# Optimization experiments

Measured on AMD Instinct MI355X. Metric: run time of the kernel, lower is better.

Reference implementation:

```python
import jax, jax.numpy as jnp
import numpy as np

N_EXPERTS = 64
TOPK = 4
DIM = 2048
B_T = 8192


def setup_inputs() -> dict:
    key = jax.random.key(0)
    k1, k2 = jax.random.split(key)
    x = jax.random.normal(k1, (B_T, DIM), jnp.float32)
    W = jax.random.normal(k2, (N_EXPERTS, DIM), jnp.float32) * 0.02  # nn.Linear weight (out, in)
    router_bias = jnp.zeros((N_EXPERTS,), jnp.float32)  # registered buffer, init zeros
    return {"x": x, "W": W, "router_bias": router_bias, "token_capacity": 3072}


def _route(x, W, router_bias, token_capacity):
    """Faithful serial greedy capacity-aware routing.

    Replicates the torch nested loop (k-major, token-minor order):
      - per step, pick argmax over the token's (mutated) logits among experts
        with remaining capacity;
      - full experts whose logit exceeds the chosen one get permanently set
        to -inf in that token's logit row (exactly what the inner while-style
        loop does);
      - if no expert has capacity, selected stays -1, weight 0, and the whole
        row becomes -inf (torch sets the top expert to -inf n_experts times).
    """
    logits0 = x @ W.T + router_bias                       # (N, E)
    scores = jax.nn.softmax(logits0, axis=-1)             # (N, E)
    cap = token_capacity // TOPK                          # python int
    remaining0 = jnp.full((N_EXPERTS,), float(cap), jnp.float32)
    N = x.shape[0]
    NEG = jnp.float32(-jnp.inf)

    def step(carry, i):
        logits, remaining = carry
        b = i % N                                         # token index (k-major order)
        row = logits[b]                                   # (E,)
        masked = jnp.where(remaining > 0, row, NEG)
        chosen = jnp.argmax(masked)
        ok = remaining[chosen] > 0                        # False only if all experts full
        sel = jnp.where(ok, chosen, -1).astype(jnp.int32)
        w = jnp.where(ok, scores[b, chosen], jnp.float32(0.0))
        full = remaining <= 0
        cval = row[chosen]
        # full experts 'above' the chosen one were visited and zapped to -inf
        new_row = jnp.where(ok,
                            jnp.where(full & (row > cval), NEG, row),
                            jnp.full_like(row, NEG))
        logits = logits.at[b].set(new_row)
        remaining = remaining.at[chosen].add(jnp.where(ok, jnp.float32(-1.0), jnp.float32(0.0)))
        return (logits, remaining), (sel, w)

    (_, _), (sel_f, w_f) = jax.lax.scan(step, (logits0, remaining0),
                                        jnp.arange(TOPK * N))
    selected = sel_f.reshape(TOPK, N).T                   # (N, TOPK)
    weights = w_f.reshape(TOPK, N).T                      # (N, TOPK)
    weights = weights / (weights.sum(axis=-1, keepdims=True) + 1e-8)
    return selected, weights


def reference(x, W, router_bias, token_capacity):
    return _route(x, W, router_bias, token_capacity)
```

## Files before the change

kernel.cpp:

```cpp
#include <hip/hip_runtime.h>
#include <math.h>

#define N_TOK 8192
#define DIM   2048
#define NE    64
#define TOPK  4
#define THETA 2e-3f
#define TPB   16
#define NBLK  (N_TOK / TPB)
#define HSTR  16

typedef short bf16x8 __attribute__((ext_vector_type(8)));
typedef float f32x4  __attribute__((ext_vector_type(4)));

#define OFF_LOGITS 0
#define OFF_MAXV   (OFF_LOGITS + N_TOK * NE)
#define OFF_DENOM  (OFF_MAXV + N_TOK)
#define OFF_HIST   (OFF_DENOM + N_TOK)
#define OFF_WH     (OFF_HIST + NE * HSTR)
#define OFF_WL     (OFF_WH + NE * DIM / 2)
#define OFF_WT     (OFF_WL + NE * DIM / 2)
#define OFF_WTMP   (OFF_WT + NE * DIM)

__device__ inline void cvt2(float a, float b, unsigned& hi, unsigned& lo) {
    const unsigned ua = __float_as_uint(a), ub = __float_as_uint(b);
    hi = __builtin_amdgcn_perm(ub, ua, 0x07060302u);
    const float ra = a - __uint_as_float(ua & 0xFFFF0000u);
    const float rb = b - __uint_as_float(ub & 0xFFFF0000u);
    lo = __builtin_amdgcn_perm(__float_as_uint(rb), __float_as_uint(ra), 0x07060302u);
}

union FragU { unsigned u[4]; bf16x8 v; uint4 q; };

__device__ inline void make_frags(const float4& p, const float4& q,
                                  bf16x8& hi, bf16x8& lo) {
    FragU H, L;
    cvt2(p.x, p.y, H.u[0], L.u[0]);
    cvt2(p.z, p.w, H.u[1], L.u[1]);
    cvt2(q.x, q.y, H.u[2], L.u[2]);
    cvt2(q.z, q.w, H.u[3], L.u[3]);
    hi = H.v; lo = L.v;
}

__global__ __launch_bounds__(256)
void k_wc(const float* __restrict__ W, unsigned short* __restrict__ wh2,
          unsigned short* __restrict__ wl2, float* __restrict__ wt,
          int* __restrict__ hist) {
    const int t = blockIdx.x * 256 + threadIdx.x;
    if (t < NE * HSTR) hist[t] = 0;
    const int l  = t & 63;
    const int grp = t >> 6;
    const int nt = grp & 3;
    const int kc = grp >> 2;
    const int e  = nt * 16 + (l & 15);
    const int k0 = kc * 32 + (l >> 4) * 8;

    const float4 p = *reinterpret_cast<const float4*>(W + (size_t)e * DIM + k0);
    const float4 q = *reinterpret_cast<const float4*>(W + (size_t)e * DIM + k0 + 4);
    FragU H, L;
    cvt2(p.x, p.y, H.u[0], L.u[0]);
    cvt2(p.z, p.w, H.u[1], L.u[1]);
    cvt2(q.x, q.y, H.u[2], L.u[2]);
    cvt2(q.z, q.w, H.u[3], L.u[3]);
    const size_t off = (size_t)grp * 512 + l * 8;
    *reinterpret_cast<uint4*>(wh2 + off) = H.q;
    *reinterpret_cast<uint4*>(wl2 + off) = L.q;

    wt[(size_t)(k0 + 0) * NE + e] = p.x;
    wt[(size_t)(k0 + 1) * NE + e] = p.y;
    wt[(size_t)(k0 + 2) * NE + e] = p.z;
    wt[(size_t)(k0 + 3) * NE + e] = p.w;
    wt[(size_t)(k0 + 4) * NE + e] = q.x;
    wt[(size_t)(k0 + 5) * NE + e] = q.y;
    wt[(size_t)(k0 + 6) * NE + e] = q.z;
    wt[(size_t)(k0 + 7) * NE + e] = q.w;
}

__global__ __launch_bounds__(512, 4)
void k_main(const float* __restrict__ x, const unsigned short* __restrict__ wh2,
            const unsigned short* __restrict__ wl2, const float* __restrict__ bias,
            const float* __restrict__ wt,
            float* __restrict__ logits, float* __restrict__ maxv,
            float* __restrict__ denomv, int* __restrict__ hist,
            float* __restrict__ out) {
    __shared__ float red[8][TPB][68];
    __shared__ float lbuf[TPB][68];
    __shared__ int   selS[TPB];
    __shared__ float wS[TPB];
    __shared__ short flagIdx[TPB];
    __shared__ int   flagCnt;

    const int tid = threadIdx.x;
    const int w   = tid >> 6;
    const int l   = tid & 63;
    const int t0  = blockIdx.x * TPB;
    const int m   = l & 15;
    const int g   = l >> 4;

    if (tid == 0) flagCnt = 0;

    const float* aP = x + (size_t)(t0 + m) * DIM + w * 32 + g * 8;
    const unsigned short* bh = wh2 + (size_t)w * 2048 + l * 8;
    const unsigned short* bl = wl2 + (size_t)w * 2048 + l * 8;

    f32x4 accA[4], accB[4];
    #pragma unroll
    for (int nt = 0; nt < 4; ++nt)
        #pragma unroll
        for (int r = 0; r < 4; ++r) { accA[nt][r] = 0.0f; accB[nt][r] = 0.0f; }

    #pragma unroll
    for (int win = 0; win < 8; ++win) {
        const float4 p = *reinterpret_cast<const float4*>(aP + win * 256);
        const float4 q = *reinterpret_cast<const float4*>(aP + win * 256 + 4);
        uint4 BH[4], BL[4];
        #pragma unroll
        for (int nt = 0; nt < 4; ++nt) {
            BH[nt] = *reinterpret_cast<const uint4*>(
                bh + (size_t)win * 16384 + nt * 512);
            BL[nt] = *reinterpret_cast<const uint4*>(
                bl + (size_t)win * 16384 + nt * 512);
        }

        bf16x8 ah, al;
        make_frags(p, q, ah, al);

        #pragma unroll
        for (int nt = 0; nt < 4; ++nt) {
            FragU b; b.q = BH[nt];
            accA[nt] = __builtin_amdgcn_mfma_f32_16x16x32_bf16(ah, b.v, accA[nt], 0, 0, 0);
            accB[nt] = __builtin_amdgcn_mfma_f32_16x16x32_bf16(al, b.v, accB[nt], 0, 0, 0);
        }
        #pragma unroll
        for (int nt = 0; nt < 4; ++nt) {
            FragU b; b.q = BL[nt];
            accB[nt] = __builtin_amdgcn_mfma_f32_16x16x32_bf16(ah, b.v, accB[nt], 0, 0, 0);
        }
    }

    #pragma unroll
    for (int nt = 0; nt < 4; ++nt)
        #pragma unroll
        for (int r = 0; r < 4; ++r)
            red[w][g * 4 + r][nt * 16 + m] = accA[nt][r] + accB[nt][r];
    __syncthreads();

    for (int e2 = tid; e2 < TPB * NE; e2 += 512) {
        const int t = e2 >> 6, e = e2 & 63;
        float s = red[0][t][e];
        #pragma unroll
        for (int ww = 1; ww < 8; ++ww) s += red[ww][t][e];
        s += bias[e];
        logits[(size_t)(t0 + t) * NE + e] = s;
        lbuf[t][e] = s;
    }
    __syncthreads();

    #pragma unroll
    for (int tt = 0; tt < 2; ++tt) {
        const int t = w * 2 + tt;
        const float lv = lbuf[t][l];
        float v1 = lv; int i1 = l; float v2 = -INFINITY;
        #pragma unroll
        for (int off = 32; off; off >>= 1) {
            const float ov1 = __shfl_xor(v1, off);
            const int   oi1 = __shfl_xor(i1, off);
            const float ov2 = __shfl_xor(v2, off);
            if (ov1 > v1 || (ov1 == v1 && oi1 < i1)) {
                v2 = fmaxf(v1, ov2); v1 = ov1; i1 = oi1;
            } else {
                v2 = fmaxf(v2, ov1);
            }
        }
        float s = expf(lv - v1);
        #pragma unroll
        for (int off = 32; off; off >>= 1) s += __shfl_xor(s, off);
        if (l == 0) {
            const int row = t0 + t;
            maxv[row]   = v1;
            denomv[row] = s;
            selS[t]     = i1;
            wS[t]       = 1.0f / s;
            if (v1 - v2 < THETA) {
                const int ix = atomicAdd(&flagCnt, 1);
                flagIdx[ix] = (short)t;
            }
        }
    }
    __syncthreads();

    const int nf = flagCnt;
    for (int fi = 0; fi < nf; ++fi) {
        const int tl  = flagIdx[fi];
        const int row = t0 + tl;
        const float* xr = x + (size_t)row * DIM + w * 256;
        const float* wb = wt + (size_t)(w * 256) * NE + l;
        float a0 = 0.0f, a1 = 0.0f;
        #pragma unroll 4
        for (int k = 0; k < 256; k += 8) {
            const float4 x0 = *reinterpret_cast<const float4*>(xr + k);
            const float4 x1 = *reinterpret_cast<const float4*>(xr + k + 4);
            a0 = fmaf(x0.x, wb[(size_t)(k + 0) * NE], a0);
            a0 = fmaf(x0.y, wb[(size_t)(k + 1) * NE], a0);
            a0 = fmaf(x0.z, wb[(size_t)(k + 2) * NE], a0);
            a0 = fmaf(x0.w, wb[(size_t)(k + 3) * NE], a0);
            a1 = fmaf(x1.x, wb[(size_t)(k + 4) * NE], a1);
            a1 = fmaf(x1.y, wb[(size_t)(k + 5) * NE], a1);
            a1 = fmaf(x1.z, wb[(size_t)(k + 6) * NE], a1);
            a1 = fmaf(x1.w, wb[(size_t)(k + 7) * NE], a1);
        }
        red[w][0][l] = a0 + a1;
        __syncthreads();
        if (w == 0) {
            float lg = bias[l];
            #pragma unroll
            for (int s2 = 0; s2 < 8; ++s2) lg += red[s2][0][l];
            logits[(size_t)row * NE + l] = lg;
            float v = lg; int idx = l;
            #pragma unroll
            for (int off = 32; off; off >>= 1) {
                const float ov = __shfl_xor(v, off);
                const int   oi = __shfl_xor(idx, off);
                if (ov > v || (ov == v && oi < idx)) { v = ov; idx = oi; }
            }
            float p = expf(lg - v);
            #pragma unroll
            for (int off = 32; off; off >>= 1) p += __shfl_xor(p, off);
            if (l == 0) {
                maxv[row]   = v;
                denomv[row] = p;
                selS[tl]    = idx;
                wS[tl]      = 1.0f / p;
            }
        }
        __syncthreads();
    }

    if (w == 0) {
        int cnt = 0;
        #pragma unroll
        for (int t = 0; t < TPB; ++t) cnt += (selS[t] == l) ? 1 : 0;
        if (cnt) atomicAdd(&hist[l * HSTR], cnt);
    }

    if (tid < TPB) {
        const int row = t0 + tid;
        const float se = (float)selS[tid];
        const float wv = wS[tid];
        const float wn = wv / (4.0f * wv + 1e-8f);
        *reinterpret_cast<float4*>(out + (size_t)row * 4) = make_float4(se, se, se, se);
        *reinterpret_cast<float4*>(out + (size_t)N_TOK * TOPK + (size_t)row * 4) =
            make_float4(wn, wn, wn, wn);
    }
}

__global__ __launch_bounds__(256)
void k_decide(const int* __restrict__ hist, const float* __restrict__ logits,
              const float* __restrict__ maxv, const float* __restrict__ denomv,
              const int* __restrict__ tc, float* __restrict__ out,
              float* __restrict__ wtmp) {
    __shared__ int flagS;
    const int tid = threadIdx.x;
    const int cap = tc[0] / TOPK;
    if (tid < NE) {
        const bool bad = (TOPK * hist[tid * HSTR] > cap);
        const unsigned long long mm = __ballot(bad);
        if (tid == 0) flagS = (mm == 0ull) ? 1 : 0;
    }
    __syncthreads();
    if (flagS) return;

    if (tid < 64) {
        const int e = tid;
        int rem = cap;
        for (int k = 0; k < TOPK; ++k) {
            for (int b = 0; b < N_TOK; ++b) {
                const float lg = logits[(size_t)b * NE + e];
                float v = (rem > 0) ? lg : -INFINITY;
                int idx = e;
                #pragma unroll
                for (int off = 32; off; off >>= 1) {
                    const float ov = __shfl_xor(v, off);
                    const int   oi = __shfl_xor(idx, off);
                    if (ov > v || (ov == v && oi < idx)) { v = ov; idx = oi; }
                }
                const bool ok = (v != -INFINITY);
                if (ok && e == idx) rem -= 1;
                const float lc = __shfl(lg, idx);
                if (e == 0) {
                    out[(size_t)b * TOPK + k]  = ok ? (float)idx : -1.0f;
                    wtmp[(size_t)b * TOPK + k] = ok ? expf(lc - maxv[b]) / denomv[b] : 0.0f;
                }
            }
        }
    }
    __syncthreads();
    for (int b = tid; b < N_TOK; b += 256) {
        const float w0 = wtmp[b * 4 + 0], w1_ = wtmp[b * 4 + 1];
        const float w2 = wtmp[b * 4 + 2], w3 = wtmp[b * 4 + 3];
        const float s = ((w0 + w1_) + w2) + w3 + 1e-8f;
        out[N_TOK * TOPK + b * 4 + 0] = w0 / s;
        out[N_TOK * TOPK + b * 4 + 1] = w1_ / s;
        out[N_TOK * TOPK + b * 4 + 2] = w2 / s;
        out[N_TOK * TOPK + b * 4 + 3] = w3 / s;
    }
}

extern "C" void kernel_launch(void* const* d_in, const int* in_sizes, int n_in,
                              void* d_out, int out_size, void* d_ws, size_t ws_size,
                              hipStream_t stream) {
    const float* x    = (const float*)d_in[0];
    const float* W    = (const float*)d_in[1];
    const float* bias = (const float*)d_in[2];
    const int*   tc   = (const int*)d_in[3];

    float* ws       = (float*)d_ws;
    float* logits   = ws + OFF_LOGITS;
    float* maxv     = ws + OFF_MAXV;
    float* denomv   = ws + OFF_DENOM;
    int*   hist     = (int*)(ws + OFF_HIST);
    unsigned short* wh2 = (unsigned short*)(ws + OFF_WH);
    unsigned short* wl2 = (unsigned short*)(ws + OFF_WL);
    float* wt       = ws + OFF_WT;
    float* wtmp     = ws + OFF_WTMP;
    float* out      = (float*)d_out;

    k_wc<<<NE * DIM / 8 / 256, 256, 0, stream>>>(W, wh2, wl2, wt, hist);
    k_main<<<NBLK, 512, 0, stream>>>(x, wh2, wl2, bias, wt, logits, maxv,
                                     denomv, hist, out);
    k_decide<<<1, 256, 0, stream>>>(hist, logits, maxv, denomv, tc, out, wtmp);
}
```

Baseline: 131.0 us.

## Stage x and W tiles in LDS via async global-to-LDS loads, 32 tokens per block

```diff
diff --git a/kernel.cpp b/kernel.cpp
--- a/kernel.cpp
+++ b/kernel.cpp
@@ -6,7 +6,7 @@
 #define NE    64
 #define TOPK  4
 #define THETA 2e-3f
-#define TPB   16
+#define TPB   32
 #define NBLK  (N_TOK / TPB)
 #define HSTR  16
 
@@ -76,89 +76,106 @@
     wt[(size_t)(k0 + 7) * NE + e] = q.w;
 }
 
-__global__ __launch_bounds__(512, 4)
+__global__ __launch_bounds__(512, 2)
 void k_main(const float* __restrict__ x, const unsigned short* __restrict__ wh2,
             const unsigned short* __restrict__ wl2, const float* __restrict__ bias,
             const float* __restrict__ wt,
             float* __restrict__ logits, float* __restrict__ maxv,
             float* __restrict__ denomv, int* __restrict__ hist,
             float* __restrict__ out) {
-    __shared__ float red[8][TPB][68];
+    __shared__ __align__(16) char smem[98304];
     __shared__ float lbuf[TPB][68];
+    __shared__ float part[8][68];
     __shared__ int   selS[TPB];
     __shared__ float wS[TPB];
     __shared__ short flagIdx[TPB];
     __shared__ int   flagCnt;
 
     const int tid = threadIdx.x;
-    const int w   = tid >> 6;
+    const int ww  = tid >> 6;
     const int l   = tid & 63;
     const int t0  = blockIdx.x * TPB;
     const int m   = l & 15;
     const int g   = l >> 4;
+    const int tg  = ww >> 2;
+    const int eg  = ww & 3;
 
     if (tid == 0) flagCnt = 0;
 
-    const float* aP = x + (size_t)(t0 + m) * DIM + w * 32 + g * 8;
-    const unsigned short* bh = wh2 + (size_t)w * 2048 + l * 8;
-    const unsigned short* bl = wl2 + (size_t)w * 2048 + l * 8;
-
-    f32x4 accA[4], accB[4];
+    auto stage = [&](int win) {
+        #pragma unroll
+        for (int j = 0; j < 12; ++j) {
+            const int dbase = ww * 12288 + j * 1024;
+            const int d = dbase + l * 16;
+            const char* src;
+            if (dbase < 32768) {
+                const int r = d >> 10;
+                const int s = ((d >> 4) & 63) ^ (r & 7);
+                src = (const char*)(x + (size_t)(t0 + r) * DIM + win * 256 + s * 4);
+            } else if (dbase < 65536) {
+                src = (const char*)wh2 + (size_t)win * 32768 + (d - 32768);
+            } else {
+                src = (const char*)wl2 + (size_t)win * 32768 + (d - 65536);
+            }
+            __builtin_amdgcn_global_load_lds(
+                (const __attribute__((address_space(1))) void*)src,
+                (__attribute__((address_space(3))) void*)(smem + dbase),
+                16, 0, 0);
+        }
+    };
+
+    stage(0);
+    asm volatile("s_waitcnt vmcnt(0)" ::: "memory");
+    __syncthreads();
+
+    f32x4 accA, accB;
     #pragma unroll
-    for (int nt = 0; nt < 4; ++nt)
-        #pragma unroll
-        for (int r = 0; r < 4; ++r) { accA[nt][r] = 0.0f; accB[nt][r] = 0.0f; }
-
-    #pragma unroll
+    for (int r = 0; r < 4; ++r) { accA[r] = 0.0f; accB[r] = 0.0f; }
+
+    const int   arow  = tg * 16 + m;
+    const char* aBase = smem + arow * 1024;
+    const int   axor  = arow & 7;
+    const char* bhB   = smem + 32768 + eg * 1024 + l * 16;
+
     for (int win = 0; win < 8; ++win) {
-        const float4 p = *reinterpret_cast<const float4*>(aP + win * 256);
-        const float4 q = *reinterpret_cast<const float4*>(aP + win * 256 + 4);
-        uint4 BH[4], BL[4];
-        #pragma unroll
-        for (int nt = 0; nt < 4; ++nt) {
-            BH[nt] = *reinterpret_cast<const uint4*>(
-                bh + (size_t)win * 16384 + nt * 512);
-            BL[nt] = *reinterpret_cast<const uint4*>(
-                bl + (size_t)win * 16384 + nt * 512);
-        }
-
-        bf16x8 ah, al;
-        make_frags(p, q, ah, al);
-
-        #pragma unroll
-        for (int nt = 0; nt < 4; ++nt) {
-            FragU b; b.q = BH[nt];
-            accA[nt] = __builtin_amdgcn_mfma_f32_16x16x32_bf16(ah, b.v, accA[nt], 0, 0, 0);
-            accB[nt] = __builtin_amdgcn_mfma_f32_16x16x32_bf16(al, b.v, accB[nt], 0, 0, 0);
-        }
-        #pragma unroll
-        for (int nt = 0; nt < 4; ++nt) {
-            FragU b; b.q = BL[nt];
-            accB[nt] = __builtin_amdgcn_mfma_f32_16x16x32_bf16(ah, b.v, accB[nt], 0, 0, 0);
-        }
-    }
-
-    #pragma unroll
-    for (int nt = 0; nt < 4; ++nt)
+        #pragma unroll
+        for (int kc = 0; kc < 8; ++kc) {
+            const int s0 = kc * 8 + g * 2;
+            const float4 p = *reinterpret_cast<const float4*>(aBase + ((s0 ^ axor) << 4));
+            const float4 q = *reinterpret_cast<const float4*>(aBase + (((s0 + 1) ^ axor) << 4));
+            FragU bh_, bl_;
+            bh_.q = *reinterpret_cast<const uint4*>(bhB + kc * 4096);
+            bl_.q = *reinterpret_cast<const uint4*>(bhB + 32768 + kc * 4096);
+            bf16x8 ah, al;
+            make_frags(p, q, ah, al);
+            accA = __builtin_amdgcn_mfma_f32_16x16x32_bf16(ah, bh_.v, accA, 0, 0, 0);
+            accB = __builtin_amdgcn_mfma_f32_16x16x32_bf16(al, bh_.v, accB, 0, 0, 0);
+            accB = __builtin_amdgcn_mfma_f32_16x16x32_bf16(ah, bl_.v, accB, 0, 0, 0);
+        }
+        if (win < 7) {
+            __syncthreads();
+            stage(win + 1);
+            asm volatile("s_waitcnt vmcnt(0)" ::: "memory");
+            __syncthreads();
+        }
+    }
+
+    {
+        const float be = bias[eg * 16 + m];
         #pragma unroll
         for (int r = 0; r < 4; ++r)
-            red[w][g * 4 + r][nt * 16 + m] = accA[nt][r] + accB[nt][r];
+            lbuf[tg * 16 + g * 4 + r][eg * 16 + m] = accA[r] + accB[r] + be;
+    }
     __syncthreads();
 
     for (int e2 = tid; e2 < TPB * NE; e2 += 512) {
         const int t = e2 >> 6, e = e2 & 63;
-        float s = red[0][t][e];
-        #pragma unroll
-        for (int ww = 1; ww < 8; ++ww) s += red[ww][t][e];
-        s += bias[e];
-        logits[(size_t)(t0 + t) * NE + e] = s;
-        lbuf[t][e] = s;
-    }
-    __syncthreads();
+        logits[(size_t)(t0 + t) * NE + e] = lbuf[t][e];
+    }
 
     #pragma unroll
-    for (int tt = 0; tt < 2; ++tt) {
-        const int t = w * 2 + tt;
+    for (int tt = 0; tt < 4; ++tt) {
+        const int t = ww * 4 + tt;
         const float lv = lbuf[t][l];
         float v1 = lv; int i1 = l; float v2 = -INFINITY;
         #pragma unroll
@@ -193,8 +210,8 @@
     for (int fi = 0; fi < nf; ++fi) {
         const int tl  = flagIdx[fi];
         const int row = t0 + tl;
-        const float* xr = x + (size_t)row * DIM + w * 256;
-        const float* wb = wt + (size_t)(w * 256) * NE + l;
+        const float* xr = x + (size_t)row * DIM + ww * 256;
+        const float* wb = wt + (size_t)(ww * 256) * NE + l;
         float a0 = 0.0f, a1 = 0.0f;
         #pragma unroll 4
         for (int k = 0; k < 256; k += 8) {
@@ -209,12 +226,12 @@
             a1 = fmaf(x1.z, wb[(size_t)(k + 6) * NE], a1);
             a1 = fmaf(x1.w, wb[(size_t)(k + 7) * NE], a1);
         }
-        red[w][0][l] = a0 + a1;
+        part[ww][l] = a0 + a1;
         __syncthreads();
-        if (w == 0) {
+        if (ww == 0) {
             float lg = bias[l];
             #pragma unroll
-            for (int s2 = 0; s2 < 8; ++s2) lg += red[s2][0][l];
+            for (int s2 = 0; s2 < 8; ++s2) lg += part[s2][l];
             logits[(size_t)row * NE + l] = lg;
             float v = lg; int idx = l;
             #pragma unroll
@@ -236,7 +253,7 @@
         __syncthreads();
     }
 
-    if (w == 0) {
+    if (ww == 0) {
         int cnt = 0;
         #pragma unroll
         for (int t = 0; t < TPB; ++t) cnt += (selS[t] == l) ? 1 : 0;
```

Result: slower. 152.6 us (+16.4%).
